# Kernel tuning notes

Hardware: AMD Instinct MI355X
Metric: run time of the kernel (lower is better)

## Reference

```python
import jax, jax.numpy as jnp
import numpy as np

N_USERS = 100000
N_ITEMS = 50000
N_NODES = N_USERS + N_ITEMS
NNZ = 2400000
EMB_DIM = 64
N_LAYERS = 3
BATCH = 16384
REG = 1e-5


def setup_inputs() -> dict:
    key = jax.random.key(0)
    ks = jax.random.split(key, 12)
    return {
        "adj_row": jax.random.randint(ks[0], (NNZ,), 0, N_NODES, dtype=jnp.int32),
        "adj_col": jax.random.randint(ks[1], (NNZ,), 0, N_NODES, dtype=jnp.int32),
        "adj_val": jax.random.uniform(ks[2], (NNZ,), dtype=jnp.float32),
        "user_emb": jax.random.normal(ks[3], (N_USERS, EMB_DIM), dtype=jnp.float32) * 0.1,
        "item_emb": jax.random.normal(ks[4], (N_ITEMS, EMB_DIM), dtype=jnp.float32) * 0.1,
        "W1": jax.random.normal(ks[5], (N_LAYERS, EMB_DIM, EMB_DIM), dtype=jnp.float32) * 0.1,
        "b1": jax.random.normal(ks[6], (N_LAYERS, EMB_DIM), dtype=jnp.float32) * 0.1,
        "W2": jax.random.normal(ks[7], (N_LAYERS, EMB_DIM, EMB_DIM), dtype=jnp.float32) * 0.1,
        "b2": jax.random.normal(ks[8], (N_LAYERS, EMB_DIM), dtype=jnp.float32) * 0.1,
        "u": jax.random.randint(ks[9], (BATCH,), 0, N_USERS, dtype=jnp.int32),
        "i": jax.random.randint(ks[10], (BATCH,), 0, N_ITEMS, dtype=jnp.int32),
        "j": jax.random.randint(ks[11], (BATCH,), 0, N_ITEMS, dtype=jnp.int32),
    }


def _spmm(row, col, val, x):
    # sparse.mm(L, x): gather source rows, scale by edge value, scatter-add to dest
    msgs = val[:, None] * x[col]  # [nnz, d]
    return jax.ops.segment_sum(msgs, row, num_segments=N_NODES)


def reference(adj_row, adj_col, adj_val, user_emb, item_emb, W1, b1, W2, b2, u, i, j):
    ego = jnp.concatenate([user_emb, item_emb], axis=0)  # [N, d]
    finals = [ego]
    for k in range(N_LAYERS):
        side_L = _spmm(adj_row, adj_col, adj_val, ego)      # L @ ego
        side_LI = side_L + ego                               # (L + I) @ ego
        simple = side_LI @ W1[k] + b1[k]
        inter = (ego * side_L) @ W2[k] + b2[k]
        ego = jax.nn.leaky_relu(simple + inter, negative_slope=0.01)
        # mess_dropout = 0 -> identity; F.normalize(p=2, dim=1, eps=1e-12)
        nrm = jnp.linalg.norm(ego, axis=1, keepdims=True)
        finals.append(ego / jnp.maximum(nrm, 1e-12))
    final = jnp.concatenate(finals, axis=1)  # [N, d*(L+1)]
    u_f, i_f = final[:N_USERS], final[N_USERS:]
    u_emb = u_f[u]
    p_emb = i_f[i]
    n_emb = i_f[j]
    y_ui = jnp.sum(u_emb * p_emb, axis=1)
    y_uj = jnp.sum(u_emb * n_emb, axis=1)
    bpr_loss = -jnp.mean(jax.nn.log_sigmoid(y_ui - y_uj))
    l2norm = (jnp.sum(u_emb ** 2) / 2.0 + jnp.sum(p_emb ** 2) / 2.0 + jnp.sum(n_emb ** 2) / 2.0) / u_emb.shape[0]
    return bpr_loss + REG * l2norm
```

## Files before the change

kernel.cpp:

```cpp
#include <hip/hip_runtime.h>

#define N_USERS 100000
#define N_ITEMS 50000
#define N_NODES 150000
#define NNZ     2400000
#define EMB     64
#define NLAYERS 3
#define BATCH   16384
#define REG     1e-5f

#define NTILES ((N_NODES + 63) / 64)

#define ROWS_PER_BUCKET 256
#define NB_BUCKET ((N_NODES + ROWS_PER_BUCKET - 1) / ROWS_PER_BUCKET)
#define BIN_CHUNK 4096
#define BIN_NB ((NNZ + BIN_CHUNK - 1) / BIN_CHUNK)
#define BCAP 6144

typedef __attribute__((ext_vector_type(8))) short bfrag8;
typedef __attribute__((ext_vector_type(4))) float vf4;

__device__ inline unsigned short f2bf(float x) {
    unsigned int u = __builtin_bit_cast(unsigned int, x);
    return (unsigned short)((u + 0x7fffu + ((u >> 16) & 1u)) >> 16);
}
__device__ inline float bf2f(unsigned short h) {
    unsigned int u = ((unsigned int)h) << 16;
    return __builtin_bit_cast(float, u);
}

__global__ void init_ego_kernel(const float4* __restrict__ ue,
                                const float4* __restrict__ ie,
                                ushort4* __restrict__ ego_bf) {
    const int n4u = N_USERS * (EMB / 4);
    const int n4  = N_NODES * (EMB / 4);
    for (int t = blockIdx.x * blockDim.x + threadIdx.x; t < n4;
         t += gridDim.x * blockDim.x) {
        float4 v = (t < n4u) ? ue[t] : ie[t - n4u];
        ushort4 h;
        h.x = f2bf(v.x); h.y = f2bf(v.y); h.z = f2bf(v.z); h.w = f2bf(v.w);
        ego_bf[t] = h;
    }
}

__global__ __launch_bounds__(256) void prep_w_kernel(
    const float* __restrict__ W1, const float* __restrict__ W2,
    unsigned short* __restrict__ BT) {
    int idx = blockIdx.x * blockDim.x + threadIdx.x;
    if (idx >= NLAYERS * 64 * 128) return;
    int l = idx / 8192;
    int rem = idx - l * 8192;
    int j = rem >> 7;
    int k = rem & 127;
    float w = (k < 64) ? W1[l * 4096 + k * 64 + j]
                       : W2[l * 4096 + (k - 64) * 64 + j];
    BT[idx] = f2bf(w);
}

__global__ __launch_bounds__(1024) void binscatter_kernel(
    const int* __restrict__ row, const int* __restrict__ col,
    const float* __restrict__ val, int* __restrict__ bcnt,
    int2* __restrict__ stage) {
    __shared__ int hist[NB_BUCKET];
    __shared__ int wbase[NB_BUCKET];
    const int t = threadIdx.x;
    const int s = blockIdx.x * BIN_CHUNK;
    const int e = min(s + BIN_CHUNK, NNZ);

    for (int b = t; b < NB_BUCKET; b += 1024) hist[b] = 0;
    __syncthreads();
    for (int i = s + t; i < e; i += 1024)
        atomicAdd(&hist[row[i] >> 8], 1);
    __syncthreads();
    for (int b = t; b < NB_BUCKET; b += 1024) {
        int c = hist[b];
        wbase[b] = c ? atomicAdd(&bcnt[b], c) : 0;
        hist[b] = 0;
    }
    __syncthreads();
    for (int i = s + t; i < e; i += 1024) {
        int r = row[i];
        int b = r >> 8;
        int off = atomicAdd(&hist[b], 1);
        stage[(size_t)b * BCAP + wbase[b] + off] =
            make_int2(col[i] | ((r & 255) << 18),
                      __builtin_bit_cast(int, val[i]));
    }
}

__global__ __launch_bounds__(1024) void bscan_kernel(
    const int* __restrict__ bcnt, int* __restrict__ bbase) {
    __shared__ int sc[1024];
    const int t = threadIdx.x;
    int v = (t < NB_BUCKET) ? bcnt[t] : 0;
    sc[t] = v;
    __syncthreads();
    int x = v;
    for (int off = 1; off < 1024; off <<= 1) {
        int y = (t >= off) ? sc[t - off] : 0;
        __syncthreads();
        x += y;
        sc[t] = x;
        __syncthreads();
    }
    if (t < NB_BUCKET) bbase[t] = x - v;
    if (t == 0) bbase[NB_BUCKET] = NNZ;
}

__global__ __launch_bounds__(1024) void bucket_place_kernel(
    const int2* __restrict__ stage, const int* __restrict__ bcnt,
    const int* __restrict__ bbase, int* __restrict__ rp,
    int2* __restrict__ sce) {
    __shared__ int cnt[ROWS_PER_BUCKET];
    __shared__ int sc[ROWS_PER_BUCKET];
    __shared__ int cur[ROWS_PER_BUCKET];
    const int b = blockIdx.x;
    const int t = threadIdx.x;
    const int row0 = b * ROWS_PER_BUCKET;
    const size_t S0 = (size_t)b * BCAP;
    const int ne = bcnt[b];
    const int B0 = bbase[b];
    if (t < 256) cnt[t] = 0;
    __syncthreads();
    for (int i = t; i < ne; i += 1024)
        atomicAdd(&cnt[(stage[S0 + i].x >> 18) & 255], 1);
    __syncthreads();
    int v = 0, x = 0;
    if (t < 256) { v = cnt[t]; x = v; sc[t] = v; }
    __syncthreads();
    for (int off = 1; off < 256; off <<= 1) {
        int y = (t < 256 && t >= off) ? sc[t - off] : 0;
        __syncthreads();
        if (t < 256) { x += y; sc[t] = x; }
        __syncthreads();
    }
    if (t < 256) {
        int excl = x - v;
        int row = row0 + t;
        if (row <= N_NODES) rp[row] = B0 + excl;
        cur[t] = B0 + excl;
    }
    __syncthreads();
    for (int i = t; i < ne; i += 1024) {
        int2 pk = stage[S0 + i];
        int rl = (pk.x >> 18) & 255;
        int pos = atomicAdd(&cur[rl], 1);
        sce[pos] = make_int2(pk.x & 0x3FFFF, pk.y);
    }
}

__global__ __launch_bounds__(256) void spmm_csr_kernel(
    const int* __restrict__ rp, const int2* __restrict__ sce,
    const unsigned short* __restrict__ ego_bf,
    unsigned short* __restrict__ side_bf) {
    const int lane = threadIdx.x & 63;
    const int q    = lane >> 4;
    const int ql   = lane & 15;
    int r = (blockIdx.x * blockDim.x + threadIdx.x) >> 6;
    if (r >= N_NODES) return;
    const uint2* egoV = (const uint2*)ego_bf;
    int s = rp[r], e = rp[r + 1];
    float a0 = 0.f, a1 = 0.f, a2 = 0.f, a3 = 0.f;
    int k = s;
    for (; k + 15 < e; k += 16) {
        int2 c0 = sce[k + q];
        int2 c1 = sce[k + 4 + q];
        int2 c2 = sce[k + 8 + q];
        int2 c3 = sce[k + 12 + q];
        uint2 g0 = egoV[(size_t)c0.x * 16 + ql];
        uint2 g1 = egoV[(size_t)c1.x * 16 + ql];
        uint2 g2 = egoV[(size_t)c2.x * 16 + ql];
        uint2 g3 = egoV[(size_t)c3.x * 16 + ql];
        float w0 = __builtin_bit_cast(float, c0.y);
        float w1 = __builtin_bit_cast(float, c1.y);
        float w2 = __builtin_bit_cast(float, c2.y);
        float w3 = __builtin_bit_cast(float, c3.y);
        a0 = fmaf(w0, bf2f((unsigned short)(g0.x & 0xffffu)), a0);
        a1 = fmaf(w0, bf2f((unsigned short)(g0.x >> 16)), a1);
        a2 = fmaf(w0, bf2f((unsigned short)(g0.y & 0xffffu)), a2);
        a3 = fmaf(w0, bf2f((unsigned short)(g0.y >> 16)), a3);
        a0 = fmaf(w1, bf2f((unsigned short)(g1.x & 0xffffu)), a0);
        a1 = fmaf(w1, bf2f((unsigned short)(g1.x >> 16)), a1);
        a2 = fmaf(w1, bf2f((unsigned short)(g1.y & 0xffffu)), a2);
        a3 = fmaf(w1, bf2f((unsigned short)(g1.y >> 16)), a3);
        a0 = fmaf(w2, bf2f((unsigned short)(g2.x & 0xffffu)), a0);
        a1 = fmaf(w2, bf2f((unsigned short)(g2.x >> 16)), a1);
        a2 = fmaf(w2, bf2f((unsigned short)(g2.y & 0xffffu)), a2);
        a3 = fmaf(w2, bf2f((unsigned short)(g2.y >> 16)), a3);
        a0 = fmaf(w3, bf2f((unsigned short)(g3.x & 0xffffu)), a0);
        a1 = fmaf(w3, bf2f((unsigned short)(g3.x >> 16)), a1);
        a2 = fmaf(w3, bf2f((unsigned short)(g3.y & 0xffffu)), a2);
        a3 = fmaf(w3, bf2f((unsigned short)(g3.y >> 16)), a3);
    }
    if (k + 7 < e) {
        int2 c0 = sce[k + q];
        int2 c1 = sce[k + 4 + q];
        uint2 g0 = egoV[(size_t)c0.x * 16 + ql];
        uint2 g1 = egoV[(size_t)c1.x * 16 + ql];
        float w0 = __builtin_bit_cast(float, c0.y);
        float w1 = __builtin_bit_cast(float, c1.y);
        a0 = fmaf(w0, bf2f((unsigned short)(g0.x & 0xffffu)), a0);
        a1 = fmaf(w0, bf2f((unsigned short)(g0.x >> 16)), a1);
        a2 = fmaf(w0, bf2f((unsigned short)(g0.y & 0xffffu)), a2);
        a3 = fmaf(w0, bf2f((unsigned short)(g0.y >> 16)), a3);
        a0 = fmaf(w1, bf2f((unsigned short)(g1.x & 0xffffu)), a0);
        a1 = fmaf(w1, bf2f((unsigned short)(g1.x >> 16)), a1);
        a2 = fmaf(w1, bf2f((unsigned short)(g1.y & 0xffffu)), a2);
        a3 = fmaf(w1, bf2f((unsigned short)(g1.y >> 16)), a3);
        k += 8;
    }
    if (k + 3 < e) {
        int2 c0 = sce[k + q];
        uint2 g0 = egoV[(size_t)c0.x * 16 + ql];
        float w0 = __builtin_bit_cast(float, c0.y);
        a0 = fmaf(w0, bf2f((unsigned short)(g0.x & 0xffffu)), a0);
        a1 = fmaf(w0, bf2f((unsigned short)(g0.x >> 16)), a1);
        a2 = fmaf(w0, bf2f((unsigned short)(g0.y & 0xffffu)), a2);
        a3 = fmaf(w0, bf2f((unsigned short)(g0.y >> 16)), a3);
        k += 4;
    }
    if (k < e) {
        int idx = k + q;
        bool ok = idx < e;
        int2 c = sce[ok ? idx : (e - 1)];
        float w = ok ? __builtin_bit_cast(float, c.y) : 0.f;
        uint2 g = egoV[(size_t)c.x * 16 + ql];
        a0 = fmaf(w, bf2f((unsigned short)(g.x & 0xffffu)), a0);
        a1 = fmaf(w, bf2f((unsigned short)(g.x >> 16)), a1);
        a2 = fmaf(w, bf2f((unsigned short)(g.y & 0xffffu)), a2);
        a3 = fmaf(w, bf2f((unsigned short)(g.y >> 16)), a3);
    }
    a0 += __shfl_xor(a0, 32, 64); a0 += __shfl_xor(a0, 16, 64);
    a1 += __shfl_xor(a1, 32, 64); a1 += __shfl_xor(a1, 16, 64);
    a2 += __shfl_xor(a2, 32, 64); a2 += __shfl_xor(a2, 16, 64);
    a3 += __shfl_xor(a3, 32, 64); a3 += __shfl_xor(a3, 16, 64);
    if (q == 0) {
        uint2 o;
        o.x = (unsigned)f2bf(a0) | ((unsigned)f2bf(a1) << 16);
        o.y = (unsigned)f2bf(a2) | ((unsigned)f2bf(a3) << 16);
        ((uint2*)side_bf)[(size_t)r * 16 + ql] = o;
    }
}

__global__ __launch_bounds__(256) void gemm_dense_kernel(
    unsigned short* __restrict__ ego,
    const unsigned short* __restrict__ side_bf,
    const unsigned short* __restrict__ BT, const float* __restrict__ b1,
    const float* __restrict__ b2, float* __restrict__ nrm) {
    __shared__ unsigned short A_lds[64][136];
    const int tid  = threadIdx.x;
    const int lane = tid & 63, wm = tid >> 6;
    const int m = lane & 15, g = lane >> 4;
    const int base = blockIdx.x * 64;

    bfrag8 b[4][4];
#pragma unroll
    for (int nt = 0; nt < 4; ++nt)
#pragma unroll
        for (int kt = 0; kt < 4; ++kt)
            b[nt][kt] =
                *(const bfrag8*)(BT + (nt * 16 + m) * 128 + kt * 32 + g * 8);

    float bias[4];
#pragma unroll
    for (int nt = 0; nt < 4; ++nt)
        bias[nt] = b1[nt * 16 + m] + b2[nt * 16 + m];

#pragma unroll
    for (int it = 0; it < 2; ++it) {
        int idx = it * 256 + tid;
        int n = idx >> 3, c = idx & 7;
        int node = base + n;
        uint4 ev = make_uint4(0, 0, 0, 0), sv = make_uint4(0, 0, 0, 0);
        if (node < N_NODES) {
            ev = ((const uint4*)ego)[(size_t)node * 8 + c];
            sv = ((const uint4*)side_bf)[(size_t)node * 8 + c];
        }
        unsigned evu[4] = {ev.x, ev.y, ev.z, ev.w};
        unsigned svu[4] = {sv.x, sv.y, sv.z, sv.w};
        unsigned qv[4], pq[4];
#pragma unroll
        for (int j = 0; j < 4; ++j) {
            float e0 = bf2f((unsigned short)(evu[j] & 0xffffu));
            float e1 = bf2f((unsigned short)(evu[j] >> 16));
            float s0 = bf2f((unsigned short)(svu[j] & 0xffffu));
            float s1 = bf2f((unsigned short)(svu[j] >> 16));
            qv[j] = f2bf(e0 + s0) | ((unsigned)f2bf(e1 + s1) << 16);
            pq[j] = f2bf(e0 * s0) | ((unsigned)f2bf(e1 * s1) << 16);
        }
        *(uint4*)&A_lds[n][c * 8]      = make_uint4(qv[0], qv[1], qv[2], qv[3]);
        *(uint4*)&A_lds[n][64 + c * 8] = make_uint4(pq[0], pq[1], pq[2], pq[3]);
    }
    __syncthreads();

    bfrag8 a[4];
#pragma unroll
    for (int kt = 0; kt < 4; ++kt)
        a[kt] = *(const bfrag8*)&A_lds[wm * 16 + m][kt * 32 + g * 8];

    vf4 acc[4];
#pragma unroll
    for (int nt = 0; nt < 4; ++nt) acc[nt] = (vf4){0.f, 0.f, 0.f, 0.f};
#pragma unroll
    for (int kt = 0; kt < 4; ++kt)
#pragma unroll
        for (int nt = 0; nt < 4; ++nt)
            acc[nt] = __builtin_amdgcn_mfma_f32_16x16x32_bf16(
                a[kt], b[nt][kt], acc[nt], 0, 0, 0);

    float o[4][4];
    float sq[4] = {0.f, 0.f, 0.f, 0.f};
#pragma unroll
    for (int nt = 0; nt < 4; ++nt)
#pragma unroll
        for (int r = 0; r < 4; ++r) {
            float v = acc[nt][r] + bias[nt];
            v = (v >= 0.f) ? v : 0.01f * v;
            o[nt][r] = v;
            sq[r] += v * v;
        }
#pragma unroll
    for (int r = 0; r < 4; ++r)
#pragma unroll
        for (int off = 1; off < 16; off <<= 1)
            sq[r] += __shfl_xor(sq[r], off, 64);

#pragma unroll
    for (int r = 0; r < 4; ++r) {
        int row = base + wm * 16 + g * 4 + r;
        if (row < N_NODES) {
#pragma unroll
            for (int nt = 0; nt < 4; ++nt)
                ego[(size_t)row * 64 + nt * 16 + m] = f2bf(o[nt][r]);
            if (m == 0) nrm[row] = fmaxf(sqrtf(sq[r]), 1e-12f);
        }
    }
}

__global__ __launch_bounds__(256) void batch_kernel(
    const unsigned short* __restrict__ ego_bf, const float* __restrict__ nrm,
    int use_nrm, const int* __restrict__ u, const int* __restrict__ pi,
    const int* __restrict__ ni, float* __restrict__ dot_ui,
    float* __restrict__ dot_uj, float* __restrict__ l2b) {
    const int lane = threadIdx.x & 63;
    int b = (blockIdx.x * blockDim.x + threadIdx.x) >> 6;
    if (b >= BATCH) return;
    int un = u[b];
    int pn = N_USERS + pi[b];
    int nn = N_USERS + ni[b];
    float fu = bf2f(ego_bf[(size_t)un * EMB + lane]);
    float fp = bf2f(ego_bf[(size_t)pn * EMB + lane]);
    float fn_ = bf2f(ego_bf[(size_t)nn * EMB + lane]);
    if (use_nrm) {
        fu /= nrm[un];
        fp /= nrm[pn];
        fn_ /= nrm[nn];
    }
    float dup = fu * fp;
    float dun = fu * fn_;
    float l2  = fu * fu + fp * fp + fn_ * fn_;
#pragma unroll
    for (int off = 32; off; off >>= 1) {
        dup += __shfl_xor(dup, off, 64);
        dun += __shfl_xor(dun, off, 64);
        l2  += __shfl_xor(l2, off, 64);
    }
    if (lane == 0) {
        dot_ui[b] += dup;
        dot_uj[b] += dun;
        l2b[b]    += l2;
    }
}

__global__ __launch_bounds__(256) void loss_partial_kernel(
    const float* __restrict__ dot_ui, const float* __restrict__ dot_uj,
    const float* __restrict__ l2b, float* __restrict__ partial) {
    __shared__ float sl[256], s2[256];
    const int t = threadIdx.x;
    const int b = blockIdx.x * 256 + t;
    float x = dot_ui[b] - dot_uj[b];
    float sp = (x > 0.f) ? log1pf(expf(-x)) : (-x + log1pf(expf(x)));
    sl[t] = sp;
    s2[t] = l2b[b];
    __syncthreads();
    for (int off = 128; off; off >>= 1) {
        if (t < off) {
            sl[t] += sl[t + off];
            s2[t] += s2[t + off];
        }
        __syncthreads();
    }
    if (t == 0) {
        partial[blockIdx.x]      = sl[0];
        partial[64 + blockIdx.x] = s2[0];
    }
}

__global__ void loss_final_kernel(const float* __restrict__ partial,
                                  float* __restrict__ out) {
    const int t = threadIdx.x;
    float sp = partial[t];
    float l2 = partial[64 + t];
#pragma unroll
    for (int off = 32; off; off >>= 1) {
        sp += __shfl_down(sp, off, 64);
        l2 += __shfl_down(l2, off, 64);
    }
    if (t == 0)
        out[0] = sp / (float)BATCH + REG * (l2 * 0.5f / (float)BATCH);
}

extern "C" void kernel_launch(void* const* d_in, const int* in_sizes, int n_in,
                              void* d_out, int out_size, void* d_ws,
                              size_t ws_size, hipStream_t stream) {
    const int*   adj_row  = (const int*)d_in[0];
    const int*   adj_col  = (const int*)d_in[1];
    const float* adj_val  = (const float*)d_in[2];
    const float* user_emb = (const float*)d_in[3];
    const float* item_emb = (const float*)d_in[4];
    const float* W1       = (const float*)d_in[5];
    const float* b1       = (const float*)d_in[6];
    const float* W2       = (const float*)d_in[7];
    const float* b2       = (const float*)d_in[8];
    const int*   u        = (const int*)d_in[9];
    const int*   ii       = (const int*)d_in[10];
    const int*   jj       = (const int*)d_in[11];

    char* p = (char*)d_ws;
    auto alloc = [&](size_t bytes) {
        char* q = p;
        p += (bytes + 255) & ~(size_t)255;
        return q;
    };
    unsigned short* ego    = (unsigned short*)alloc((size_t)N_NODES * EMB * 2);
    unsigned short* side_bf= (unsigned short*)alloc((size_t)N_NODES * EMB * 2);
    int2*           sce    = (int2*)alloc((size_t)NNZ * 8);
    int2*           stage  = (int2*)alloc((size_t)NB_BUCKET * BCAP * 8);
    int*            rp     = (int*)alloc((size_t)(N_NODES + 1) * 4);
    int*            bcnt   = (int*)alloc((size_t)NB_BUCKET * 4);
    int*            bbase  = (int*)alloc((size_t)(NB_BUCKET + 1) * 4);
    float*          nrm    = (float*)alloc((size_t)N_NODES * 4);
    float*          dot_ui = (float*)alloc((size_t)BATCH * 4);
    float*          dot_uj = (float*)alloc((size_t)BATCH * 4);
    float*          l2b    = (float*)alloc((size_t)BATCH * 4);
    float*          partial= (float*)alloc(128 * 4);
    unsigned short* BT     = (unsigned short*)alloc((size_t)NLAYERS * 8192 * 2);

    hipMemsetAsync(dot_ui, 0, BATCH * sizeof(float), stream);
    hipMemsetAsync(dot_uj, 0, BATCH * sizeof(float), stream);
    hipMemsetAsync(l2b, 0, BATCH * sizeof(float), stream);
    hipMemsetAsync(bcnt, 0, NB_BUCKET * sizeof(int), stream);

    prep_w_kernel<<<(NLAYERS * 8192 + 255) / 256, 256, 0, stream>>>(W1, W2, BT);

    binscatter_kernel<<<BIN_NB, 1024, 0, stream>>>(adj_row, adj_col, adj_val,
                                                   bcnt, stage);
    bscan_kernel<<<1, 1024, 0, stream>>>(bcnt, bbase);
    bucket_place_kernel<<<NB_BUCKET, 1024, 0, stream>>>(stage, bcnt, bbase, rp,
                                                        sce);

    init_ego_kernel<<<2048, 256, 0, stream>>>((const float4*)user_emb,
                                              (const float4*)item_emb,
                                              (ushort4*)ego);

    batch_kernel<<<BATCH / 4, 256, 0, stream>>>(ego, nrm, 0, u, ii, jj,
                                                dot_ui, dot_uj, l2b);

    for (int k = 0; k < NLAYERS; ++k) {
        spmm_csr_kernel<<<(N_NODES * 64 + 255) / 256, 256, 0, stream>>>(
            rp, sce, ego, side_bf);
        gemm_dense_kernel<<<NTILES, 256, 0, stream>>>(
            ego, side_bf, BT + (size_t)k * 8192, b1 + (size_t)k * EMB,
            b2 + (size_t)k * EMB, nrm);
        batch_kernel<<<BATCH / 4, 256, 0, stream>>>(ego, nrm, 1, u, ii, jj,
                                                    dot_ui, dot_uj, l2b);
    }

    loss_partial_kernel<<<BATCH / 256, 256, 0, stream>>>(dot_ui, dot_uj, l2b,
                                                         partial);
    loss_final_kernel<<<1, 64, 0, stream>>>(partial, (float*)d_out);
}
```

Before: 373.1 us.

## Gather SpMM source embeddings from scaled FP8 copy instead of bf16

Keeps a second copy of the node embeddings in FP8 (scaled by 16), written by the init and dense GEMM kernels, and has the SpMM gather 4 bytes per lane instead of 8. The result is unscaled before being stored as bf16. This halves the random-gather traffic that dominates SpMM, but adds an extra FP8 write per layer and loses precision in the message passing. The ego layout is also permuted so each lane holds strided dimensions, and the weight prep reorders rows to match.

```diff
diff --git a/kernel.cpp b/kernel.cpp
--- a/kernel.cpp
+++ b/kernel.cpp
@@ -17,8 +17,13 @@
 #define BIN_NB ((NNZ + BIN_CHUNK - 1) / BIN_CHUNK)
 #define BCAP 6144
 
+#define F8_SCALE 16.0f
+#define F8_INV   0.0625f
+
 typedef __attribute__((ext_vector_type(8))) short bfrag8;
 typedef __attribute__((ext_vector_type(4))) float vf4;
+typedef __attribute__((ext_vector_type(2))) float f32x2;
+
 
 __device__ inline unsigned short f2bf(float x) {
     unsigned int u = __builtin_bit_cast(unsigned int, x);
@@ -29,18 +34,24 @@
     return __builtin_bit_cast(float, u);
 }
 
-__global__ void init_ego_kernel(const float4* __restrict__ ue,
-                                const float4* __restrict__ ie,
-                                ushort4* __restrict__ ego_bf) {
-    const int n4u = N_USERS * (EMB / 4);
-    const int n4  = N_NODES * (EMB / 4);
-    for (int t = blockIdx.x * blockDim.x + threadIdx.x; t < n4;
-         t += gridDim.x * blockDim.x) {
-        float4 v = (t < n4u) ? ue[t] : ie[t - n4u];
-        ushort4 h;
-        h.x = f2bf(v.x); h.y = f2bf(v.y); h.z = f2bf(v.z); h.w = f2bf(v.w);
-        ego_bf[t] = h;
-    }
+__global__ __launch_bounds__(256) void init_ego_kernel(
+    const float* __restrict__ ue, const float* __restrict__ ie,
+    unsigned short* __restrict__ ego_bf, unsigned char* __restrict__ ego_f8) {
+    int idx = blockIdx.x * 256 + threadIdx.x;
+    if (idx >= N_NODES * 16) return;
+    int row = idx >> 4, q = idx & 15;
+    const float* src = (row < N_USERS)
+                           ? ue + (size_t)row * 64
+                           : ie + (size_t)(row - N_USERS) * 64;
+    float v0 = src[q], v1 = src[16 + q], v2 = src[32 + q], v3 = src[48 + q];
+    uint2 o;
+    o.x = (unsigned)f2bf(v0) | ((unsigned)f2bf(v1) << 16);
+    o.y = (unsigned)f2bf(v2) | ((unsigned)f2bf(v3) << 16);
+    ((uint2*)ego_bf)[(size_t)row * 16 + q] = o;
+    int u = __builtin_amdgcn_cvt_pk_fp8_f32(v0 * F8_SCALE, v1 * F8_SCALE, 0,
+                                            false);
+    u = __builtin_amdgcn_cvt_pk_fp8_f32(v2 * F8_SCALE, v3 * F8_SCALE, u, true);
+    ((int*)ego_f8)[(size_t)row * 16 + q] = u;
 }
 
 __global__ __launch_bounds__(256) void prep_w_kernel(
@@ -52,8 +63,10 @@
     int rem = idx - l * 8192;
     int j = rem >> 7;
     int k = rem & 127;
-    float w = (k < 64) ? W1[l * 4096 + k * 64 + j]
-                       : W2[l * 4096 + (k - 64) * 64 + j];
+    int p = k & 63;
+    int d = ((p & 3) << 4) | (p >> 2);
+    float w = (k < 64) ? W1[l * 4096 + d * 64 + j]
+                       : W2[l * 4096 + d * 64 + j];
     BT[idx] = f2bf(w);
 }
 
@@ -151,72 +164,56 @@
 
 __global__ __launch_bounds__(256) void spmm_csr_kernel(
     const int* __restrict__ rp, const int2* __restrict__ sce,
-    const unsigned short* __restrict__ ego_bf,
+    const unsigned char* __restrict__ ego_f8,
     unsigned short* __restrict__ side_bf) {
     const int lane = threadIdx.x & 63;
     const int q    = lane >> 4;
     const int ql   = lane & 15;
     int r = (blockIdx.x * blockDim.x + threadIdx.x) >> 6;
     if (r >= N_NODES) return;
-    const uint2* egoV = (const uint2*)ego_bf;
+    const int* egoF = (const int*)ego_f8;
     int s = rp[r], e = rp[r + 1];
     float a0 = 0.f, a1 = 0.f, a2 = 0.f, a3 = 0.f;
     int k = s;
+#define F8_ACC(gi, wi)                                                       \
+    {                                                                        \
+        f32x2 lo_ = __builtin_amdgcn_cvt_pk_f32_fp8(gi, false);              \
+        f32x2 hi_ = __builtin_amdgcn_cvt_pk_f32_fp8(gi, true);               \
+        a0 = fmaf(wi, lo_.x, a0);                                            \
+        a1 = fmaf(wi, lo_.y, a1);                                            \
+        a2 = fmaf(wi, hi_.x, a2);                                            \
+        a3 = fmaf(wi, hi_.y, a3);                                            \
+    }
     for (; k + 15 < e; k += 16) {
         int2 c0 = sce[k + q];
         int2 c1 = sce[k + 4 + q];
         int2 c2 = sce[k + 8 + q];
         int2 c3 = sce[k + 12 + q];
-        uint2 g0 = egoV[(size_t)c0.x * 16 + ql];
-        uint2 g1 = egoV[(size_t)c1.x * 16 + ql];
-        uint2 g2 = egoV[(size_t)c2.x * 16 + ql];
-        uint2 g3 = egoV[(size_t)c3.x * 16 + ql];
+        int g0 = egoF[(size_t)c0.x * 16 + ql];
+        int g1 = egoF[(size_t)c1.x * 16 + ql];
+        int g2 = egoF[(size_t)c2.x * 16 + ql];
+        int g3 = egoF[(size_t)c3.x * 16 + ql];
         float w0 = __builtin_bit_cast(float, c0.y);
         float w1 = __builtin_bit_cast(float, c1.y);
         float w2 = __builtin_bit_cast(float, c2.y);
         float w3 = __builtin_bit_cast(float, c3.y);
-        a0 = fmaf(w0, bf2f((unsigned short)(g0.x & 0xffffu)), a0);
-        a1 = fmaf(w0, bf2f((unsigned short)(g0.x >> 16)), a1);
-        a2 = fmaf(w0, bf2f((unsigned short)(g0.y & 0xffffu)), a2);
-        a3 = fmaf(w0, bf2f((unsigned short)(g0.y >> 16)), a3);
-        a0 = fmaf(w1, bf2f((unsigned short)(g1.x & 0xffffu)), a0);
-        a1 = fmaf(w1, bf2f((unsigned short)(g1.x >> 16)), a1);
-        a2 = fmaf(w1, bf2f((unsigned short)(g1.y & 0xffffu)), a2);
-        a3 = fmaf(w1, bf2f((unsigned short)(g1.y >> 16)), a3);
-        a0 = fmaf(w2, bf2f((unsigned short)(g2.x & 0xffffu)), a0);
-        a1 = fmaf(w2, bf2f((unsigned short)(g2.x >> 16)), a1);
-        a2 = fmaf(w2, bf2f((unsigned short)(g2.y & 0xffffu)), a2);
-        a3 = fmaf(w2, bf2f((unsigned short)(g2.y >> 16)), a3);
-        a0 = fmaf(w3, bf2f((unsigned short)(g3.x & 0xffffu)), a0);
-        a1 = fmaf(w3, bf2f((unsigned short)(g3.x >> 16)), a1);
-        a2 = fmaf(w3, bf2f((unsigned short)(g3.y & 0xffffu)), a2);
-        a3 = fmaf(w3, bf2f((unsigned short)(g3.y >> 16)), a3);
+        F8_ACC(g0, w0) F8_ACC(g1, w1) F8_ACC(g2, w2) F8_ACC(g3, w3)
     }
     if (k + 7 < e) {
         int2 c0 = sce[k + q];
         int2 c1 = sce[k + 4 + q];
-        uint2 g0 = egoV[(size_t)c0.x * 16 + ql];
-        uint2 g1 = egoV[(size_t)c1.x * 16 + ql];
+        int g0 = egoF[(size_t)c0.x * 16 + ql];
+        int g1 = egoF[(size_t)c1.x * 16 + ql];
         float w0 = __builtin_bit_cast(float, c0.y);
         float w1 = __builtin_bit_cast(float, c1.y);
-        a0 = fmaf(w0, bf2f((unsigned short)(g0.x & 0xffffu)), a0);
-        a1 = fmaf(w0, bf2f((unsigned short)(g0.x >> 16)), a1);
-        a2 = fmaf(w0, bf2f((unsigned short)(g0.y & 0xffffu)), a2);
-        a3 = fmaf(w0, bf2f((unsigned short)(g0.y >> 16)), a3);
-        a0 = fmaf(w1, bf2f((unsigned short)(g1.x & 0xffffu)), a0);
-        a1 = fmaf(w1, bf2f((unsigned short)(g1.x >> 16)), a1);
-        a2 = fmaf(w1, bf2f((unsigned short)(g1.y & 0xffffu)), a2);
-        a3 = fmaf(w1, bf2f((unsigned short)(g1.y >> 16)), a3);
+        F8_ACC(g0, w0) F8_ACC(g1, w1)
         k += 8;
     }
     if (k + 3 < e) {
         int2 c0 = sce[k + q];
-        uint2 g0 = egoV[(size_t)c0.x * 16 + ql];
+        int g0 = egoF[(size_t)c0.x * 16 + ql];
         float w0 = __builtin_bit_cast(float, c0.y);
-        a0 = fmaf(w0, bf2f((unsigned short)(g0.x & 0xffffu)), a0);
-        a1 = fmaf(w0, bf2f((unsigned short)(g0.x >> 16)), a1);
-        a2 = fmaf(w0, bf2f((unsigned short)(g0.y & 0xffffu)), a2);
-        a3 = fmaf(w0, bf2f((unsigned short)(g0.y >> 16)), a3);
+        F8_ACC(g0, w0)
         k += 4;
     }
     if (k < e) {
@@ -224,17 +221,16 @@
         bool ok = idx < e;
         int2 c = sce[ok ? idx : (e - 1)];
         float w = ok ? __builtin_bit_cast(float, c.y) : 0.f;
-        uint2 g = egoV[(size_t)c.x * 16 + ql];
-        a0 = fmaf(w, bf2f((unsigned short)(g.x & 0xffffu)), a0);
-        a1 = fmaf(w, bf2f((unsigned short)(g.x >> 16)), a1);
-        a2 = fmaf(w, bf2f((unsigned short)(g.y & 0xffffu)), a2);
-        a3 = fmaf(w, bf2f((unsigned short)(g.y >> 16)), a3);
-    }
+        int g = egoF[(size_t)c.x * 16 + ql];
+        F8_ACC(g, w)
+    }
+#undef F8_ACC
     a0 += __shfl_xor(a0, 32, 64); a0 += __shfl_xor(a0, 16, 64);
     a1 += __shfl_xor(a1, 32, 64); a1 += __shfl_xor(a1, 16, 64);
     a2 += __shfl_xor(a2, 32, 64); a2 += __shfl_xor(a2, 16, 64);
     a3 += __shfl_xor(a3, 32, 64); a3 += __shfl_xor(a3, 16, 64);
     if (q == 0) {
+        a0 *= F8_INV; a1 *= F8_INV; a2 *= F8_INV; a3 *= F8_INV;
         uint2 o;
         o.x = (unsigned)f2bf(a0) | ((unsigned)f2bf(a1) << 16);
         o.y = (unsigned)f2bf(a2) | ((unsigned)f2bf(a3) << 16);
@@ -244,6 +240,7 @@
 
 __global__ __launch_bounds__(256) void gemm_dense_kernel(
     unsigned short* __restrict__ ego,
+    unsigned char* __restrict__ ego_f8,
     const unsigned short* __restrict__ side_bf,
     const unsigned short* __restrict__ BT, const float* __restrict__ b1,
     const float* __restrict__ b2, float* __restrict__ nrm) {
@@ -329,9 +326,15 @@
     for (int r = 0; r < 4; ++r) {
         int row = base + wm * 16 + g * 4 + r;
         if (row < N_NODES) {
-#pragma unroll
-            for (int nt = 0; nt < 4; ++nt)
-                ego[(size_t)row * 64 + nt * 16 + m] = f2bf(o[nt][r]);
+            uint2 ob;
+            ob.x = (unsigned)f2bf(o[0][r]) | ((unsigned)f2bf(o[1][r]) << 16);
+            ob.y = (unsigned)f2bf(o[2][r]) | ((unsigned)f2bf(o[3][r]) << 16);
+            ((uint2*)ego)[(size_t)row * 16 + m] = ob;
+            int uf = __builtin_amdgcn_cvt_pk_fp8_f32(
+                o[0][r] * F8_SCALE, o[1][r] * F8_SCALE, 0, false);
+            uf = __builtin_amdgcn_cvt_pk_fp8_f32(
+                o[2][r] * F8_SCALE, o[3][r] * F8_SCALE, uf, true);
+            ((int*)ego_f8)[(size_t)row * 16 + m] = uf;
             if (m == 0) nrm[row] = fmaxf(sqrtf(sq[r]), 1e-12f);
         }
     }
@@ -433,6 +436,7 @@
         return q;
     };
     unsigned short* ego    = (unsigned short*)alloc((size_t)N_NODES * EMB * 2);
+    unsigned char*  ego_f8 = (unsigned char*)alloc((size_t)N_NODES * EMB);
     unsigned short* side_bf= (unsigned short*)alloc((size_t)N_NODES * EMB * 2);
     int2*           sce    = (int2*)alloc((size_t)NNZ * 8);
     int2*           stage  = (int2*)alloc((size_t)NB_BUCKET * BCAP * 8);
@@ -459,18 +463,17 @@
     bucket_place_kernel<<<NB_BUCKET, 1024, 0, stream>>>(stage, bcnt, bbase, rp,
                                                         sce);
 
-    init_ego_kernel<<<2048, 256, 0, stream>>>((const float4*)user_emb,
-                                              (const float4*)item_emb,
-                                              (ushort4*)ego);
+    init_ego_kernel<<<(N_NODES * 16 + 255) / 256, 256, 0, stream>>>(
+        user_emb, item_emb, ego, ego_f8);
 
     batch_kernel<<<BATCH / 4, 256, 0, stream>>>(ego, nrm, 0, u, ii, jj,
                                                 dot_ui, dot_uj, l2b);
 
     for (int k = 0; k < NLAYERS; ++k) {
         spmm_csr_kernel<<<(N_NODES * 64 + 255) / 256, 256, 0, stream>>>(
-            rp, sce, ego, side_bf);
+            rp, sce, ego_f8, side_bf);
         gemm_dense_kernel<<<NTILES, 256, 0, stream>>>(
-            ego, side_bf, BT + (size_t)k * 8192, b1 + (size_t)k * EMB,
+            ego, ego_f8, side_bf, BT + (size_t)k * 8192, b1 + (size_t)k * EMB,
             b2 + (size_t)k * EMB, nrm);
         batch_kernel<<<BATCH / 4, 256, 0, stream>>>(ego, nrm, 1, u, ii, jj,
                                                     dot_ui, dot_uj, l2b);
```

After: 368.1 us. No clear change (-1.3%).
